# Kernel optimization log

Measured on AMD Instinct MI355X. Metric: run time of the kernel, lower is better.

The kernel has to match this reference:

```python
import jax, jax.numpy as jnp
import numpy as np

N_NODES = 100000
N_EDGES = 1600000
IN_CH = 128
HID = 128
OUT_CH = 40


def setup_inputs() -> dict:
    key = jax.random.key(0)
    ks = jax.random.split(key, 8)
    x = jax.random.normal(ks[0], (N_NODES, IN_CH), dtype=jnp.float32)
    edge_index = jax.random.randint(ks[1], (2, N_EDGES), 0, N_NODES, dtype=jnp.int64)
    s1 = 1.0 / np.sqrt(IN_CH)
    s2 = 1.0 / np.sqrt(HID)
    # SAGEConv layer 1: lin_l (applied to aggregated neighbors, has bias), lin_r (applied to root, no bias)
    Wl1 = jax.random.uniform(ks[2], (IN_CH, HID), jnp.float32, -s1, s1)
    b1 = jnp.zeros((HID,), jnp.float32)
    Wr1 = jax.random.uniform(ks[3], (IN_CH, HID), jnp.float32, -s1, s1)
    # SAGEConv layer 2
    Wl2 = jax.random.uniform(ks[4], (HID, OUT_CH), jnp.float32, -s2, s2)
    b2 = jnp.zeros((OUT_CH,), jnp.float32)
    Wr2 = jax.random.uniform(ks[5], (HID, OUT_CH), jnp.float32, -s2, s2)
    return {"x": x, "edge_index": edge_index, "Wl1": Wl1, "b1": b1, "Wr1": Wr1,
            "Wl2": Wl2, "b2": b2, "Wr2": Wr2}


def _sage_conv(x, src, dst, Wl, b, Wr):
    # mean-aggregate source-node features onto target nodes (PyG SAGEConv, aggr='mean')
    msg_sum = jax.ops.segment_sum(x[src], dst, num_segments=N_NODES)  # [N, F]
    deg = jax.ops.segment_sum(jnp.ones((src.shape[0],), x.dtype), dst, num_segments=N_NODES)
    aggr = msg_sum / jnp.maximum(deg, 1.0)[:, None]
    return aggr @ Wl + b + x @ Wr


def reference(x, edge_index, Wl1, b1, Wr1, Wl2, b2, Wr2):
    src, dst = edge_index[0], edge_index[1]
    h = _sage_conv(x, src, dst, Wl1, b1, Wr1)
    h = jax.nn.relu(h)  # dropout is identity in eval mode
    h = _sage_conv(h, src, dst, Wl2, b2, Wr2)
    return jax.nn.log_softmax(h, axis=-1)
```

## Files before the change

### kernel.cpp

```cpp
#include <hip/hip_runtime.h>
#include <math.h>

#define NN 100000
#define NE 1600000
#define NBUK ((NN + 255) / 256)
#define CAP 5120
#define NBLK_A 500
#define EPB (NE / NBLK_A)
#define GPB (EPB / 4)
#define MT ((NN + 127) / 128)
#define MPAD ((size_t)MT * 128)
#define PACK_B 192
#define CVT_B0 (NBLK_A + PACK_B)
#define FRONT_GRID 2048

typedef __attribute__((ext_vector_type(8))) short short8;
typedef __attribute__((ext_vector_type(4))) float f32x4;
typedef __attribute__((ext_vector_type(4))) int i32x4;
typedef unsigned short ushort_t;
typedef unsigned int uint_t;

__device__ inline ushort_t f2bf(float f) {
    uint_t u = __builtin_bit_cast(uint_t, f);
    u += 0x7FFFu + ((u >> 16) & 1u);
    return (ushort_t)(u >> 16);
}
__device__ inline float bits2f(uint_t u) { return __builtin_bit_cast(float, u); }
__device__ inline float lo16(uint_t u) { return bits2f(u << 16); }
__device__ inline float hi16(uint_t u) { return bits2f(u & 0xFFFF0000u); }

__device__ inline void gload_lds16(const void* g, void* l) {
    __builtin_amdgcn_global_load_lds(
        (const __attribute__((address_space(1))) unsigned int*)g,
        (__attribute__((address_space(3))) unsigned int*)l, 16, 0, 0);
}

__global__ __launch_bounds__(256) void front(const float* __restrict__ x,
                                             ushort_t* __restrict__ xb,
                                             const float* __restrict__ Wl1,
                                             const float* __restrict__ Wr1,
                                             const float* __restrict__ Wl2,
                                             const float* __restrict__ Wr2,
                                             ushort_t* __restrict__ W1T,
                                             ushort_t* __restrict__ W2T,
                                             const int* __restrict__ ei,
                                             int* __restrict__ bhp) {
    __shared__ int h[NBUK];
    int bid = blockIdx.x, tid = threadIdx.x;
    if (bid < NBLK_A) {
        for (int i = tid; i < NBUK; i += 256) h[i] = 0;
        __syncthreads();
        const i32x4* dsts = (const i32x4*)(ei + NE + bid * EPB);
        for (int g = tid; g < GPB; g += 256) {
            i32x4 d = __builtin_nontemporal_load(dsts + g);
#pragma unroll
            for (int j = 0; j < 4; ++j) atomicAdd(&h[d[j] >> 8], 1);
        }
        __syncthreads();
        for (int i = tid; i < NBUK; i += 256) bhp[bid * NBUK + i] = h[i];
    } else if (bid < CVT_B0) {
        int gid = (bid - NBLK_A) * 256 + tid;
        if (gid < 256 * 128) {
            int n = gid >> 7, k = gid & 127;
            float v = (n < 128) ? Wl1[k * 128 + n] : Wr1[k * 128 + (n - 128)];
            W1T[gid] = f2bf(v);
        } else {
            int g = gid - 256 * 128;
            if (g < 128 * 128) {
                int n = g >> 7, k = g & 127;
                float v = 0.0f;
                if (n < 40)      v = Wl2[k * 40 + n];
                else if (n < 80) v = Wr2[k * 40 + (n - 40)];
                W2T[g] = f2bf(v);
            }
        }
    } else {
        const int total = NN * 128 / 8;
        const int nb = FRONT_GRID - CVT_B0;
        const f32x4* src = (const f32x4*)x;
        for (int g = (bid - CVT_B0) * 256 + tid; g < total; g += nb * 256) {
            f32x4 v0 = __builtin_nontemporal_load(src + (size_t)g * 2);
            f32x4 v1 = __builtin_nontemporal_load(src + (size_t)g * 2 + 1);
            i32x4 o;
            o[0] = ((uint_t)f2bf(v0[1]) << 16) | (uint_t)f2bf(v0[0]);
            o[1] = ((uint_t)f2bf(v0[3]) << 16) | (uint_t)f2bf(v0[2]);
            o[2] = ((uint_t)f2bf(v1[1]) << 16) | (uint_t)f2bf(v1[0]);
            o[3] = ((uint_t)f2bf(v1[3]) << 16) | (uint_t)f2bf(v1[2]);
            *(i32x4*)(xb + (size_t)g * 8) = o;
        }
    }
}

__global__ __launch_bounds__(512) void scan_buckets(const int* __restrict__ bhp,
                                                    int* __restrict__ boff,
                                                    int* __restrict__ gcur,
                                                    int* __restrict__ offsets) {
    __shared__ int part[512];
    int t = threadIdx.x;
    int v = 0;
    if (t < NBUK) {
        for (int b = 0; b < NBLK_A; ++b) v += bhp[b * NBUK + t];
    }
    part[t] = v;
    __syncthreads();
    for (int d = 1; d < 512; d <<= 1) {
        int tmp = (t >= d) ? part[t - d] : 0;
        __syncthreads();
        part[t] += tmp;
        __syncthreads();
    }
    if (t <= NBUK) {
        int excl = (t == 0) ? 0 : part[t - 1];
        boff[t] = excl;
        if (t < NBUK) gcur[t] = excl;
    }
    if (t == 0) offsets[NN] = NE;
}

__global__ __launch_bounds__(256) void bin_pass(const int* __restrict__ ei,
                                                const int* __restrict__ bhp,
                                                int* __restrict__ gcur,
                                                int* __restrict__ pairs) {
    __shared__ int h[NBUK];
    __shared__ int base[NBUK];
    int bid = blockIdx.x, tid = threadIdx.x;
    const int* myh = bhp + bid * NBUK;
    for (int i = tid; i < NBUK; i += 256) {
        int c = myh[i];
        base[i] = c ? atomicAdd(&gcur[i], c) : 0;
        h[i] = 0;
    }
    __syncthreads();
    int e0 = bid * EPB;
    const i32x4* dsts = (const i32x4*)(ei + NE + e0);
    const i32x4* srcs = (const i32x4*)(ei + e0);
    for (int g = tid; g < GPB; g += 256) {
        i32x4 d = __builtin_nontemporal_load(dsts + g);
        i32x4 s = __builtin_nontemporal_load(srcs + g);
#pragma unroll
        for (int j = 0; j < 4; ++j) {
            int buk = d[j] >> 8;
            int pos = base[buk] + atomicAdd(&h[buk], 1);
            pairs[pos] = (s[j] << 8) | (d[j] & 255);
        }
    }
}

template <int LAYER>
__device__ inline void gemm_tile(char* As, char* Bs,
                                 const ushort_t* __restrict__ A,
                                 const ushort_t* __restrict__ Bt,
                                 ushort_t* __restrict__ O0,
                                 ushort_t* __restrict__ O1,
                                 ushort_t* __restrict__ Croot,
                                 int bx, int by, int tid, int M) {
    int lane = tid & 63, wid = tid >> 6;
    int quad = lane >> 4, l15 = lane & 15;
    int wm = (wid & 1) * 64, wn = (wid >> 1) * 64;
    int mBase = bx * 128, nBase = by * 128;

    const char* aT = (const char*)(A + (size_t)mBase * 128);
    const char* bT = (const char*)(Bt + (size_t)nBase * 128);
#pragma unroll
    for (int ii = 0; ii < 8; ++ii) {
        int rr = (wid * 8 + ii) * 4 + quad;
        int src = rr * 256 + ((l15 * 16) ^ ((rr & 7) << 4));
        int ldsb = (wid * 8 + ii) * 1024;
        gload_lds16(aT + src, As + ldsb);
        gload_lds16(bT + src, Bs + ldsb);
    }
    asm volatile("s_waitcnt vmcnt(0)" ::: "memory");
    __syncthreads();

    f32x4 acc[4][4];
#pragma unroll
    for (int i = 0; i < 4; ++i)
#pragma unroll
        for (int j = 0; j < 4; ++j) acc[i][j] = (f32x4){0.f, 0.f, 0.f, 0.f};

#pragma unroll
    for (int kk = 0; kk < 4; ++kk) {
        int kByte = kk * 64 + quad * 16;
        short8 af[4], bfr[4];
#pragma unroll
        for (int i = 0; i < 4; ++i) {
            int row = wm + i * 16 + l15;
            af[i] = *(const short8*)(As + row * 256 + (kByte ^ ((row & 7) << 4)));
        }
#pragma unroll
        for (int j = 0; j < 4; ++j) {
            int row = wn + j * 16 + l15;
            bfr[j] = *(const short8*)(Bs + row * 256 + (kByte ^ ((row & 7) << 4)));
        }
#pragma unroll
        for (int i = 0; i < 4; ++i)
#pragma unroll
            for (int j = 0; j < 4; ++j)
                acc[i][j] = __builtin_amdgcn_mfma_f32_16x16x32_bf16(af[i], bfr[j],
                                                                    acc[i][j], 0, 0, 0);
    }

#pragma unroll
    for (int i = 0; i < 4; ++i) {
#pragma unroll
        for (int r = 0; r < 4; ++r) {
            int m = mBase + wm + i * 16 + quad * 4 + r;
            if (m >= M) continue;
#pragma unroll
            for (int j = 0; j < 4; ++j) {
                int n = nBase + wn + j * 16 + l15;
                float v = acc[i][j][r];
                if (LAYER == 1) {
                    if (n < 128) O0[(size_t)m * 128 + n] = f2bf(v);
                    else if (n < 256) Croot[(size_t)m * 128 + (n - 128)] = f2bf(v);
                } else {
                    if (n < 32) O0[(size_t)m * 32 + n] = f2bf(v);
                    else if (n < 40) O1[(size_t)m * 8 + (n - 32)] = f2bf(v);
                    else if (n < 80) Croot[(size_t)m * 40 + (n - 40)] = f2bf(v);
                }
            }
        }
    }
}

__global__ __launch_bounds__(256, 2) void sort_gemm1(const int* __restrict__ boff,
                                                     const int* __restrict__ pairs,
                                                     int* __restrict__ offsets,
                                                     int* __restrict__ ssrc,
                                                     const ushort_t* __restrict__ A,
                                                     const ushort_t* __restrict__ Bt,
                                                     ushort_t* __restrict__ G,
                                                     ushort_t* __restrict__ Croot) {
    __shared__ __align__(16) char smem[65536];
    int bid = blockIdx.x, tid = threadIdx.x;
    if (bid < NBUK) {
        int* plds = (int*)smem;
        int* slds = (int*)(smem + CAP * 4);
        int* cnt  = (int*)(smem + CAP * 8);
        int* excl = cnt + 256;
        int buk = bid;
        int bstart = boff[buk], bend = boff[buk + 1];
        int count = min(bend - bstart, CAP);
        int lo = buk << 8;
        cnt[tid] = 0;
        __syncthreads();
        for (int j = tid; j < count; j += 256) {
            int p = pairs[bstart + j];
            plds[j] = p;
            atomicAdd(&cnt[p & 255], 1);
        }
        __syncthreads();
        int c = cnt[tid];
        excl[tid] = c;
        __syncthreads();
        for (int d = 1; d < 256; d <<= 1) {
            int tmp = (tid >= d) ? excl[tid - d] : 0;
            __syncthreads();
            excl[tid] += tmp;
            __syncthreads();
        }
        int myExcl = excl[tid] - c;
        __syncthreads();
        excl[tid] = myExcl;
        cnt[tid] = 0;
        __syncthreads();
        for (int j = tid; j < count; j += 256) {
            int p = plds[j];
            int loc = p & 255;
            int pos = excl[loc] + atomicAdd(&cnt[loc], 1);
            slds[pos] = p >> 8;
        }
        __syncthreads();
        for (int j = tid; j < count; j += 256) ssrc[bstart + j] = slds[j];
        if (lo + tid < NN) offsets[lo + tid] = bstart + myExcl;
    } else {
        int gb = bid - NBUK;
        int bx = gb % MT, by = gb / MT;
        gemm_tile<1>(smem, smem + 32768, A, Bt, G, (ushort_t*)nullptr, Croot, bx, by, tid, NN);
    }
}

__global__ __launch_bounds__(256, 2) void gemm2_k(const ushort_t* __restrict__ A,
                                                  const ushort_t* __restrict__ Bt,
                                                  ushort_t* __restrict__ G2a,
                                                  ushort_t* __restrict__ G2b,
                                                  ushort_t* __restrict__ C2root) {
    __shared__ __align__(16) char smem[65536];
    gemm_tile<2>(smem, smem + 32768, A, Bt, G2a, G2b, C2root, blockIdx.x, 0, threadIdx.x, NN);
}

__global__ __launch_bounds__(256) void aggregate1(const int* __restrict__ offsets,
                                                  const int* __restrict__ ssrc,
                                                  const ushort_t* __restrict__ G1,
                                                  const ushort_t* __restrict__ C1root,
                                                  const float* __restrict__ b1,
                                                  ushort_t* __restrict__ s1b) {
    int w = (blockIdx.x * blockDim.x + threadIdx.x) >> 6;
    int lane = threadIdx.x & 63;
    if (w >= NN) return;
    int start = offsets[w], end = offsets[w + 1];
    int g = lane >> 4, q = lane & 15;
    const char* Gb = (const char*)G1;
    int qb = q << 4;
    float a0 = 0.f, a1 = 0.f, a2 = 0.f, a3 = 0.f, a4 = 0.f, a5 = 0.f, a6 = 0.f, a7 = 0.f;
    for (int base = start; base < end; base += 64) {
        int cnt = min(64, end - base);
        int idx = (base + lane < end) ? ssrc[base + lane] : 0;
        int j = 0;
        for (; j + 16 <= cnt; j += 16) {
            int s0 = __shfl(idx, j + g, 64);
            int s1 = __shfl(idx, j + 4 + g, 64);
            int s2 = __shfl(idx, j + 8 + g, 64);
            int s3 = __shfl(idx, j + 12 + g, 64);
            uint4 u0 = *(const uint4*)(Gb + (s0 << 8) + qb);
            uint4 u1 = *(const uint4*)(Gb + (s1 << 8) + qb);
            uint4 u2 = *(const uint4*)(Gb + (s2 << 8) + qb);
            uint4 u3 = *(const uint4*)(Gb + (s3 << 8) + qb);
            a0 += (lo16(u0.x) + lo16(u1.x)) + (lo16(u2.x) + lo16(u3.x));
            a1 += (hi16(u0.x) + hi16(u1.x)) + (hi16(u2.x) + hi16(u3.x));
            a2 += (lo16(u0.y) + lo16(u1.y)) + (lo16(u2.y) + lo16(u3.y));
            a3 += (hi16(u0.y) + hi16(u1.y)) + (hi16(u2.y) + hi16(u3.y));
            a4 += (lo16(u0.z) + lo16(u1.z)) + (lo16(u2.z) + lo16(u3.z));
            a5 += (hi16(u0.z) + hi16(u1.z)) + (hi16(u2.z) + hi16(u3.z));
            a6 += (lo16(u0.w) + lo16(u1.w)) + (lo16(u2.w) + lo16(u3.w));
            a7 += (hi16(u0.w) + hi16(u1.w)) + (hi16(u2.w) + hi16(u3.w));
        }
        for (; j + 8 <= cnt; j += 8) {
            int s0 = __shfl(idx, j + g, 64);
            int s1 = __shfl(idx, j + 4 + g, 64);
            uint4 u0 = *(const uint4*)(Gb + (s0 << 8) + qb);
            uint4 u1 = *(const uint4*)(Gb + (s1 << 8) + qb);
            a0 += lo16(u0.x) + lo16(u1.x);
            a1 += hi16(u0.x) + hi16(u1.x);
            a2 += lo16(u0.y) + lo16(u1.y);
            a3 += hi16(u0.y) + hi16(u1.y);
            a4 += lo16(u0.z) + lo16(u1.z);
            a5 += hi16(u0.z) + hi16(u1.z);
            a6 += lo16(u0.w) + lo16(u1.w);
            a7 += hi16(u0.w) + hi16(u1.w);
        }
        for (; j < cnt; j += 4) {
            int e = j + g;
            int s0 = __shfl(idx, (e < cnt) ? e : 0, 64);
            if (e < cnt) {
                uint4 u0 = *(const uint4*)(Gb + (s0 << 8) + qb);
                a0 += lo16(u0.x); a1 += hi16(u0.x);
                a2 += lo16(u0.y); a3 += hi16(u0.y);
                a4 += lo16(u0.z); a5 += hi16(u0.z);
                a6 += lo16(u0.w); a7 += hi16(u0.w);
            }
        }
    }
    a0 += __shfl_xor(a0, 16, 64); a0 += __shfl_xor(a0, 32, 64);
    a1 += __shfl_xor(a1, 16, 64); a1 += __shfl_xor(a1, 32, 64);
    a2 += __shfl_xor(a2, 16, 64); a2 += __shfl_xor(a2, 32, 64);
    a3 += __shfl_xor(a3, 16, 64); a3 += __shfl_xor(a3, 32, 64);
    a4 += __shfl_xor(a4, 16, 64); a4 += __shfl_xor(a4, 32, 64);
    a5 += __shfl_xor(a5, 16, 64); a5 += __shfl_xor(a5, 32, 64);
    a6 += __shfl_xor(a6, 16, 64); a6 += __shfl_xor(a6, 32, 64);
    a7 += __shfl_xor(a7, 16, 64); a7 += __shfl_xor(a7, 32, 64);
    if (g == 0) {
        float inv = 1.0f / fmaxf((float)(end - start), 1.0f);
        uint4 rv = *(const uint4*)((const char*)C1root + (size_t)w * 256 + qb);
        float4 c0 = *(const float4*)(b1 + q * 8);
        float4 c1 = *(const float4*)(b1 + q * 8 + 4);
        float h0 = fmaxf(a0 * inv + c0.x + lo16(rv.x), 0.f);
        float h1 = fmaxf(a1 * inv + c0.y + hi16(rv.x), 0.f);
        float h2 = fmaxf(a2 * inv + c0.z + lo16(rv.y), 0.f);
        float h3 = fmaxf(a3 * inv + c0.w + hi16(rv.y), 0.f);
        float h4 = fmaxf(a4 * inv + c1.x + lo16(rv.z), 0.f);
        float h5 = fmaxf(a5 * inv + c1.y + hi16(rv.z), 0.f);
        float h6 = fmaxf(a6 * inv + c1.z + lo16(rv.w), 0.f);
        float h7 = fmaxf(a7 * inv + c1.w + hi16(rv.w), 0.f);
        uint4 o;
        o.x = ((uint_t)f2bf(h1) << 16) | (uint_t)f2bf(h0);
        o.y = ((uint_t)f2bf(h3) << 16) | (uint_t)f2bf(h2);
        o.z = ((uint_t)f2bf(h5) << 16) | (uint_t)f2bf(h4);
        o.w = ((uint_t)f2bf(h7) << 16) | (uint_t)f2bf(h6);
        *(uint4*)((char*)s1b + (size_t)w * 256 + qb) = o;
    }
}

__global__ __launch_bounds__(256) void aggregate2(const int* __restrict__ offsets,
                                                  const int* __restrict__ ssrc,
                                                  const ushort_t* __restrict__ G2a,
                                                  const ushort_t* __restrict__ G2b,
                                                  const ushort_t* __restrict__ C2root,
                                                  const float* __restrict__ b2,
                                                  float* __restrict__ out) {
    int w = (blockIdx.x * blockDim.x + threadIdx.x) >> 6;
    int lane = threadIdx.x & 63;
    if (w >= NN) return;
    int start = offsets[w], end = offsets[w + 1];
    int g = lane >> 4, q = lane & 15;
    bool act = q < 10;
    const char* tbl;
    int rsh, off0;
    if (q < 8) { tbl = (const char*)G2a; rsh = 6; off0 = q * 8; }
    else       { tbl = (const char*)G2b; rsh = 4; off0 = (q - 8) * 8; }
    float a0 = 0.f, a1 = 0.f, a2 = 0.f, a3 = 0.f;
    for (int base = start; base < end; base += 64) {
        int cnt = min(64, end - base);
        int idx = (base + lane < end) ? ssrc[base + lane] : 0;
        int j = 0;
        for (; j + 16 <= cnt; j += 16) {
            int s0 = __shfl(idx, j + g, 64);
            int s1 = __shfl(idx, j + 4 + g, 64);
            int s2 = __shfl(idx, j + 8 + g, 64);
            int s3 = __shfl(idx, j + 12 + g, 64);
            if (act) {
                uint2 u0 = *(const uint2*)(tbl + ((size_t)s0 << rsh) + off0);
                uint2 u1 = *(const uint2*)(tbl + ((size_t)s1 << rsh) + off0);
                uint2 u2 = *(const uint2*)(tbl + ((size_t)s2 << rsh) + off0);
                uint2 u3 = *(const uint2*)(tbl + ((size_t)s3 << rsh) + off0);
                a0 += (lo16(u0.x) + lo16(u1.x)) + (lo16(u2.x) + lo16(u3.x));
                a1 += (hi16(u0.x) + hi16(u1.x)) + (hi16(u2.x) + hi16(u3.x));
                a2 += (lo16(u0.y) + lo16(u1.y)) + (lo16(u2.y) + lo16(u3.y));
                a3 += (hi16(u0.y) + hi16(u1.y)) + (hi16(u2.y) + hi16(u3.y));
            }
        }
        for (; j + 8 <= cnt; j += 8) {
            int s0 = __shfl(idx, j + g, 64);
            int s1 = __shfl(idx, j + 4 + g, 64);
            if (act) {
                uint2 u0 = *(const uint2*)(tbl + ((size_t)s0 << rsh) + off0);
                uint2 u1 = *(const uint2*)(tbl + ((size_t)s1 << rsh) + off0);
                a0 += lo16(u0.x) + lo16(u1.x);
                a1 += hi16(u0.x) + hi16(u1.x);
                a2 += lo16(u0.y) + lo16(u1.y);
                a3 += hi16(u0.y) + hi16(u1.y);
            }
        }
        for (; j < cnt; j += 4) {
            int e = j + g;
            int s0 = __shfl(idx, (e < cnt) ? e : 0, 64);
            if (act && e < cnt) {
                uint2 u0 = *(const uint2*)(tbl + ((size_t)s0 << rsh) + off0);
                a0 += lo16(u0.x); a1 += hi16(u0.x);
                a2 += lo16(u0.y); a3 += hi16(u0.y);
            }
        }
    }
    a0 += __shfl_xor(a0, 16, 64); a0 += __shfl_xor(a0, 32, 64);
    a1 += __shfl_xor(a1, 16, 64); a1 += __shfl_xor(a1, 32, 64);
    a2 += __shfl_xor(a2, 16, 64); a2 += __shfl_xor(a2, 32, 64);
    a3 += __shfl_xor(a3, 16, 64); a3 += __shfl_xor(a3, 32, 64);
    if (g == 0) {
        float inv = 1.0f / fmaxf((float)(end - start), 1.0f);
        float v0 = -INFINITY, v1 = -INFINITY, v2 = -INFINITY, v3 = -INFINITY;
        if (act) {
            uint2 rv = *(const uint2*)((const char*)C2root + (size_t)w * 80 + (q << 3));
            float4 bb = *(const float4*)(b2 + q * 4);
            v0 = a0 * inv + bb.x + lo16(rv.x);
            v1 = a1 * inv + bb.y + hi16(rv.x);
            v2 = a2 * inv + bb.z + lo16(rv.y);
            v3 = a3 * inv + bb.w + hi16(rv.y);
        }
        float m = fmaxf(fmaxf(v0, v1), fmaxf(v2, v3));
#pragma unroll
        for (int d = 8; d >= 1; d >>= 1) m = fmaxf(m, __shfl_xor(m, d, 64));
        float e = act ? (expf(v0 - m) + expf(v1 - m)) + (expf(v2 - m) + expf(v3 - m)) : 0.f;
#pragma unroll
        for (int d = 8; d >= 1; d >>= 1) e += __shfl_xor(e, d, 64);
        float lse = m + logf(e);
        if (act) {
            float4 o = make_float4(v0 - lse, v1 - lse, v2 - lse, v3 - lse);
            *(float4*)(out + (size_t)w * 40 + q * 4) = o;
        }
    }
}

extern "C" void kernel_launch(void* const* d_in, const int* in_sizes, int n_in,
                              void* d_out, int out_size, void* d_ws, size_t ws_size,
                              hipStream_t stream) {
    const float* x   = (const float*)d_in[0];
    const int*   ei  = (const int*)d_in[1];
    const float* Wl1 = (const float*)d_in[2];
    const float* b1  = (const float*)d_in[3];
    const float* Wr1 = (const float*)d_in[4];
    const float* Wl2 = (const float*)d_in[5];
    const float* b2  = (const float*)d_in[6];
    const float* Wr2 = (const float*)d_in[7];
    float* out = (float*)d_out;

    char* ws = (char*)d_ws;
    size_t off = 0;
    auto alloc = [&](size_t bytes) -> void* {
        void* p = ws + off;
        off = (off + bytes + 255) & ~(size_t)255;
        return p;
    };
    int*      boff    = (int*)alloc((size_t)(NBUK + 1) * 4);
    int*      gcur    = (int*)alloc((size_t)NBUK * 4);
    int*      bhp     = (int*)alloc((size_t)NBLK_A * NBUK * 4);
    int*      pairs   = (int*)alloc((size_t)NE * 4);
    int*      offsets = (int*)alloc((size_t)(NN + 1) * 4);
    int*      ssrc    = (int*)alloc((size_t)NE * 4);
    ushort_t* W1T     = (ushort_t*)alloc((size_t)256 * 128 * 2);
    ushort_t* W2T     = (ushort_t*)alloc((size_t)128 * 128 * 2);
    ushort_t* xb      = (ushort_t*)alloc(MPAD * 128 * 2);
    ushort_t* G1      = (ushort_t*)alloc((size_t)NN * 128 * 2);
    ushort_t* C1root  = (ushort_t*)alloc((size_t)NN * 128 * 2);
    ushort_t* s1b     = (ushort_t*)alloc(MPAD * 128 * 2);
    ushort_t* G2a     = (ushort_t*)alloc((size_t)NN * 32 * 2);
    ushort_t* G2b     = (ushort_t*)alloc((size_t)NN * 8 * 2);
    ushort_t* C2root  = (ushort_t*)alloc((size_t)NN * 40 * 2);

    front<<<FRONT_GRID, 256, 0, stream>>>(x, xb, Wl1, Wr1, Wl2, Wr2, W1T, W2T, ei, bhp);
    scan_buckets<<<1, 512, 0, stream>>>(bhp, boff, gcur, offsets);
    bin_pass<<<NBLK_A, 256, 0, stream>>>(ei, bhp, gcur, pairs);
    sort_gemm1<<<NBUK + MT * 2, 256, 0, stream>>>(boff, pairs, offsets, ssrc,
                                                  xb, W1T, G1, C1root);
    aggregate1<<<(NN * 64 + 255) / 256, 256, 0, stream>>>(offsets, ssrc, G1, C1root, b1, s1b);
    gemm2_k<<<MT, 256, 0, stream>>>(s1b, W2T, G2a, G2b, C2root);
    aggregate2<<<(NN * 64 + 255) / 256, 256, 0, stream>>>(offsets, ssrc, G2a, G2b,
                                                          C2root, b2, out);
}
```

Baseline: 326.8 us.

## Use fixed-capacity buckets and fuse layer-2 GEMM into aggregation

Edge binning now gives each bucket a fixed-capacity region (bucket*CAP). This drops the global histogram pass in front and the single-block scan kernel, and bin_pass computes its own per-block histogram. Node ranges are stored as separate start/end arrays. The layer-2 GEMM kernel is removed: each wavefront multiplies its aggregated hidden row by W2 with scalar FMAs and shuffles, which avoids writing and re-reading s1b. The cost is that edges beyond a bucket's CAP are silently dropped, and the per-node dot products on CUDA cores replace the MFMA GEMM.

```diff
diff --git a/kernel.cpp b/kernel.cpp
--- a/kernel.cpp
+++ b/kernel.cpp
@@ -11,7 +11,6 @@
 #define MT ((NN + 127) / 128)
 #define MPAD ((size_t)MT * 128)
 #define PACK_B 192
-#define CVT_B0 (NBLK_A + PACK_B)
 #define FRONT_GRID 2048
 
 typedef __attribute__((ext_vector_type(8))) short short8;
@@ -28,6 +27,7 @@
 __device__ inline float bits2f(uint_t u) { return __builtin_bit_cast(float, u); }
 __device__ inline float lo16(uint_t u) { return bits2f(u << 16); }
 __device__ inline float hi16(uint_t u) { return bits2f(u & 0xFFFF0000u); }
+__device__ inline float bf2f(ushort_t b) { return bits2f((uint_t)b << 16); }
 
 __device__ inline void gload_lds16(const void* g, void* l) {
     __builtin_amdgcn_global_load_lds(
@@ -43,23 +43,13 @@
                                              const float* __restrict__ Wr2,
                                              ushort_t* __restrict__ W1T,
                                              ushort_t* __restrict__ W2T,
-                                             const int* __restrict__ ei,
-                                             int* __restrict__ bhp) {
-    __shared__ int h[NBUK];
+                                             int* __restrict__ gcur) {
     int bid = blockIdx.x, tid = threadIdx.x;
-    if (bid < NBLK_A) {
-        for (int i = tid; i < NBUK; i += 256) h[i] = 0;
-        __syncthreads();
-        const i32x4* dsts = (const i32x4*)(ei + NE + bid * EPB);
-        for (int g = tid; g < GPB; g += 256) {
-            i32x4 d = __builtin_nontemporal_load(dsts + g);
-#pragma unroll
-            for (int j = 0; j < 4; ++j) atomicAdd(&h[d[j] >> 8], 1);
-        }
-        __syncthreads();
-        for (int i = tid; i < NBUK; i += 256) bhp[bid * NBUK + i] = h[i];
-    } else if (bid < CVT_B0) {
-        int gid = (bid - NBLK_A) * 256 + tid;
+    if (bid == 0) {
+        for (int i = tid; i < NBUK; i += 256) gcur[i] = i * CAP;
+    }
+    if (bid < PACK_B) {
+        int gid = bid * 256 + tid;
         if (gid < 256 * 128) {
             int n = gid >> 7, k = gid & 127;
             float v = (n < 128) ? Wl1[k * 128 + n] : Wr1[k * 128 + (n - 128)];
@@ -76,9 +66,9 @@
         }
     } else {
         const int total = NN * 128 / 8;
-        const int nb = FRONT_GRID - CVT_B0;
+        const int nb = FRONT_GRID - PACK_B;
         const f32x4* src = (const f32x4*)x;
-        for (int g = (bid - CVT_B0) * 256 + tid; g < total; g += nb * 256) {
+        for (int g = (bid - PACK_B) * 256 + tid; g < total; g += nb * 256) {
             f32x4 v0 = __builtin_nontemporal_load(src + (size_t)g * 2);
             f32x4 v1 = __builtin_nontemporal_load(src + (size_t)g * 2 + 1);
             i32x4 o;
@@ -91,69 +81,47 @@
     }
 }
 
-__global__ __launch_bounds__(512) void scan_buckets(const int* __restrict__ bhp,
-                                                    int* __restrict__ boff,
-                                                    int* __restrict__ gcur,
-                                                    int* __restrict__ offsets) {
-    __shared__ int part[512];
-    int t = threadIdx.x;
-    int v = 0;
-    if (t < NBUK) {
-        for (int b = 0; b < NBLK_A; ++b) v += bhp[b * NBUK + t];
-    }
-    part[t] = v;
-    __syncthreads();
-    for (int d = 1; d < 512; d <<= 1) {
-        int tmp = (t >= d) ? part[t - d] : 0;
-        __syncthreads();
-        part[t] += tmp;
-        __syncthreads();
-    }
-    if (t <= NBUK) {
-        int excl = (t == 0) ? 0 : part[t - 1];
-        boff[t] = excl;
-        if (t < NBUK) gcur[t] = excl;
-    }
-    if (t == 0) offsets[NN] = NE;
-}
-
 __global__ __launch_bounds__(256) void bin_pass(const int* __restrict__ ei,
-                                                const int* __restrict__ bhp,
                                                 int* __restrict__ gcur,
                                                 int* __restrict__ pairs) {
     __shared__ int h[NBUK];
     __shared__ int base[NBUK];
     int bid = blockIdx.x, tid = threadIdx.x;
-    const int* myh = bhp + bid * NBUK;
-    for (int i = tid; i < NBUK; i += 256) {
-        int c = myh[i];
-        base[i] = c ? atomicAdd(&gcur[i], c) : 0;
-        h[i] = 0;
-    }
+    for (int i = tid; i < NBUK; i += 256) h[i] = 0;
     __syncthreads();
     int e0 = bid * EPB;
     const i32x4* dsts = (const i32x4*)(ei + NE + e0);
     const i32x4* srcs = (const i32x4*)(ei + e0);
     for (int g = tid; g < GPB; g += 256) {
         i32x4 d = __builtin_nontemporal_load(dsts + g);
+#pragma unroll
+        for (int j = 0; j < 4; ++j) atomicAdd(&h[d[j] >> 8], 1);
+    }
+    __syncthreads();
+    for (int i = tid; i < NBUK; i += 256) {
+        int c = h[i];
+        base[i] = c ? atomicAdd(&gcur[i], c) : 0;
+        h[i] = 0;
+    }
+    __syncthreads();
+    for (int g = tid; g < GPB; g += 256) {
+        i32x4 d = __builtin_nontemporal_load(dsts + g);
         i32x4 s = __builtin_nontemporal_load(srcs + g);
 #pragma unroll
         for (int j = 0; j < 4; ++j) {
             int buk = d[j] >> 8;
             int pos = base[buk] + atomicAdd(&h[buk], 1);
-            pairs[pos] = (s[j] << 8) | (d[j] & 255);
-        }
-    }
-}
-
-template <int LAYER>
-__device__ inline void gemm_tile(char* As, char* Bs,
-                                 const ushort_t* __restrict__ A,
-                                 const ushort_t* __restrict__ Bt,
-                                 ushort_t* __restrict__ O0,
-                                 ushort_t* __restrict__ O1,
-                                 ushort_t* __restrict__ Croot,
-                                 int bx, int by, int tid, int M) {
+            if (pos < (buk + 1) * CAP) pairs[pos] = (s[j] << 8) | (d[j] & 255);
+        }
+    }
+}
+
+__device__ inline void gemm1_tile(char* As, char* Bs,
+                                  const ushort_t* __restrict__ A,
+                                  const ushort_t* __restrict__ Bt,
+                                  ushort_t* __restrict__ G,
+                                  ushort_t* __restrict__ Croot,
+                                  int bx, int by, int tid) {
     int lane = tid & 63, wid = tid >> 6;
     int quad = lane >> 4, l15 = lane & 15;
     int wm = (wid & 1) * 64, wn = (wid >> 1) * 64;
@@ -205,27 +173,22 @@
 #pragma unroll
         for (int r = 0; r < 4; ++r) {
             int m = mBase + wm + i * 16 + quad * 4 + r;
-            if (m >= M) continue;
+            if (m >= NN) continue;
 #pragma unroll
             for (int j = 0; j < 4; ++j) {
                 int n = nBase + wn + j * 16 + l15;
                 float v = acc[i][j][r];
-                if (LAYER == 1) {
-                    if (n < 128) O0[(size_t)m * 128 + n] = f2bf(v);
-                    else if (n < 256) Croot[(size_t)m * 128 + (n - 128)] = f2bf(v);
-                } else {
-                    if (n < 32) O0[(size_t)m * 32 + n] = f2bf(v);
-                    else if (n < 40) O1[(size_t)m * 8 + (n - 32)] = f2bf(v);
-                    else if (n < 80) Croot[(size_t)m * 40 + (n - 40)] = f2bf(v);
-                }
-            }
-        }
-    }
-}
-
-__global__ __launch_bounds__(256, 2) void sort_gemm1(const int* __restrict__ boff,
+                if (n < 128) G[(size_t)m * 128 + n] = f2bf(v);
+                else Croot[(size_t)m * 128 + (n - 128)] = f2bf(v);
+            }
+        }
+    }
+}
+
+__global__ __launch_bounds__(256, 2) void sort_gemm1(const int* __restrict__ gcur,
                                                      const int* __restrict__ pairs,
-                                                     int* __restrict__ offsets,
+                                                     int* __restrict__ starts,
+                                                     int* __restrict__ ends,
                                                      int* __restrict__ ssrc,
                                                      const ushort_t* __restrict__ A,
                                                      const ushort_t* __restrict__ Bt,
@@ -239,8 +202,8 @@
         int* cnt  = (int*)(smem + CAP * 8);
         int* excl = cnt + 256;
         int buk = bid;
-        int bstart = boff[buk], bend = boff[buk + 1];
-        int count = min(bend - bstart, CAP);
+        int bstart = buk * CAP;
+        int count = min(gcur[buk] - bstart, CAP);
         int lo = buk << 8;
         cnt[tid] = 0;
         __syncthreads();
@@ -272,33 +235,31 @@
         }
         __syncthreads();
         for (int j = tid; j < count; j += 256) ssrc[bstart + j] = slds[j];
-        if (lo + tid < NN) offsets[lo + tid] = bstart + myExcl;
+        if (lo + tid < NN) {
+            starts[lo + tid] = bstart + myExcl;
+            ends[lo + tid]   = bstart + myExcl + c;
+        }
     } else {
         int gb = bid - NBUK;
         int bx = gb % MT, by = gb / MT;
-        gemm_tile<1>(smem, smem + 32768, A, Bt, G, (ushort_t*)nullptr, Croot, bx, by, tid, NN);
-    }
-}
-
-__global__ __launch_bounds__(256, 2) void gemm2_k(const ushort_t* __restrict__ A,
-                                                  const ushort_t* __restrict__ Bt,
-                                                  ushort_t* __restrict__ G2a,
-                                                  ushort_t* __restrict__ G2b,
-                                                  ushort_t* __restrict__ C2root) {
-    __shared__ __align__(16) char smem[65536];
-    gemm_tile<2>(smem, smem + 32768, A, Bt, G2a, G2b, C2root, blockIdx.x, 0, threadIdx.x, NN);
-}
-
-__global__ __launch_bounds__(256) void aggregate1(const int* __restrict__ offsets,
-                                                  const int* __restrict__ ssrc,
-                                                  const ushort_t* __restrict__ G1,
-                                                  const ushort_t* __restrict__ C1root,
-                                                  const float* __restrict__ b1,
-                                                  ushort_t* __restrict__ s1b) {
+        gemm1_tile(smem, smem + 32768, A, Bt, G, Croot, bx, by, tid);
+    }
+}
+
+__global__ __launch_bounds__(256) void aggregate1f(const int* __restrict__ starts,
+                                                   const int* __restrict__ ends,
+                                                   const int* __restrict__ ssrc,
+                                                   const ushort_t* __restrict__ G1,
+                                                   const ushort_t* __restrict__ C1root,
+                                                   const float* __restrict__ b1,
+                                                   const ushort_t* __restrict__ W2T,
+                                                   ushort_t* __restrict__ G2a,
+                                                   ushort_t* __restrict__ G2b,
+                                                   ushort_t* __restrict__ C2root) {
     int w = (blockIdx.x * blockDim.x + threadIdx.x) >> 6;
     int lane = threadIdx.x & 63;
     if (w >= NN) return;
-    int start = offsets[w], end = offsets[w + 1];
+    int start = starts[w], end = ends[w];
     int g = lane >> 4, q = lane & 15;
     const char* Gb = (const char*)G1;
     int qb = q << 4;
@@ -359,29 +320,48 @@
     a5 += __shfl_xor(a5, 16, 64); a5 += __shfl_xor(a5, 32, 64);
     a6 += __shfl_xor(a6, 16, 64); a6 += __shfl_xor(a6, 32, 64);
     a7 += __shfl_xor(a7, 16, 64); a7 += __shfl_xor(a7, 32, 64);
-    if (g == 0) {
-        float inv = 1.0f / fmaxf((float)(end - start), 1.0f);
-        uint4 rv = *(const uint4*)((const char*)C1root + (size_t)w * 256 + qb);
-        float4 c0 = *(const float4*)(b1 + q * 8);
-        float4 c1 = *(const float4*)(b1 + q * 8 + 4);
-        float h0 = fmaxf(a0 * inv + c0.x + lo16(rv.x), 0.f);
-        float h1 = fmaxf(a1 * inv + c0.y + hi16(rv.x), 0.f);
-        float h2 = fmaxf(a2 * inv + c0.z + lo16(rv.y), 0.f);
-        float h3 = fmaxf(a3 * inv + c0.w + hi16(rv.y), 0.f);
-        float h4 = fmaxf(a4 * inv + c1.x + lo16(rv.z), 0.f);
-        float h5 = fmaxf(a5 * inv + c1.y + hi16(rv.z), 0.f);
-        float h6 = fmaxf(a6 * inv + c1.z + lo16(rv.w), 0.f);
-        float h7 = fmaxf(a7 * inv + c1.w + hi16(rv.w), 0.f);
-        uint4 o;
-        o.x = ((uint_t)f2bf(h1) << 16) | (uint_t)f2bf(h0);
-        o.y = ((uint_t)f2bf(h3) << 16) | (uint_t)f2bf(h2);
-        o.z = ((uint_t)f2bf(h5) << 16) | (uint_t)f2bf(h4);
-        o.w = ((uint_t)f2bf(h7) << 16) | (uint_t)f2bf(h6);
-        *(uint4*)((char*)s1b + (size_t)w * 256 + qb) = o;
-    }
-}
-
-__global__ __launch_bounds__(256) void aggregate2(const int* __restrict__ offsets,
+
+    float inv = 1.0f / fmaxf((float)(end - start), 1.0f);
+    uint4 rv = *(const uint4*)((const char*)C1root + (size_t)w * 256 + qb);
+    float4 c0 = *(const float4*)(b1 + q * 8);
+    float4 c1 = *(const float4*)(b1 + q * 8 + 4);
+    float hf0 = bf2f(f2bf(fmaxf(a0 * inv + c0.x + lo16(rv.x), 0.f)));
+    float hf1 = bf2f(f2bf(fmaxf(a1 * inv + c0.y + hi16(rv.x), 0.f)));
+    float hf2 = bf2f(f2bf(fmaxf(a2 * inv + c0.z + lo16(rv.y), 0.f)));
+    float hf3 = bf2f(f2bf(fmaxf(a3 * inv + c0.w + hi16(rv.y), 0.f)));
+    float hf4 = bf2f(f2bf(fmaxf(a4 * inv + c1.x + lo16(rv.z), 0.f)));
+    float hf5 = bf2f(f2bf(fmaxf(a5 * inv + c1.y + hi16(rv.z), 0.f)));
+    float hf6 = bf2f(f2bf(fmaxf(a6 * inv + c1.z + lo16(rv.w), 0.f)));
+    float hf7 = bf2f(f2bf(fmaxf(a7 * inv + c1.w + hi16(rv.w), 0.f)));
+
+    float accL = 0.f, accH = 0.f;
+    const ushort_t* WrowL = W2T + (size_t)lane * 128;
+    const ushort_t* WrowH = W2T + (size_t)(64 + q) * 128;
+#pragma unroll
+    for (int kq = 0; kq < 16; ++kq) {
+        float hb0 = __shfl(hf0, kq, 64), hb1 = __shfl(hf1, kq, 64);
+        float hb2 = __shfl(hf2, kq, 64), hb3 = __shfl(hf3, kq, 64);
+        float hb4 = __shfl(hf4, kq, 64), hb5 = __shfl(hf5, kq, 64);
+        float hb6 = __shfl(hf6, kq, 64), hb7 = __shfl(hf7, kq, 64);
+        short8 wl = *(const short8*)(WrowL + kq * 8);
+        short8 wh = *(const short8*)(WrowH + kq * 8);
+        accL += hb0 * bf2f((ushort_t)wl[0]) + hb1 * bf2f((ushort_t)wl[1])
+              + hb2 * bf2f((ushort_t)wl[2]) + hb3 * bf2f((ushort_t)wl[3])
+              + hb4 * bf2f((ushort_t)wl[4]) + hb5 * bf2f((ushort_t)wl[5])
+              + hb6 * bf2f((ushort_t)wl[6]) + hb7 * bf2f((ushort_t)wl[7]);
+        accH += hb0 * bf2f((ushort_t)wh[0]) + hb1 * bf2f((ushort_t)wh[1])
+              + hb2 * bf2f((ushort_t)wh[2]) + hb3 * bf2f((ushort_t)wh[3])
+              + hb4 * bf2f((ushort_t)wh[4]) + hb5 * bf2f((ushort_t)wh[5])
+              + hb6 * bf2f((ushort_t)wh[6]) + hb7 * bf2f((ushort_t)wh[7]);
+    }
+    if (lane < 32) G2a[(size_t)w * 32 + lane] = f2bf(accL);
+    else if (lane < 40) G2b[(size_t)w * 8 + (lane - 32)] = f2bf(accL);
+    else C2root[(size_t)w * 40 + (lane - 40)] = f2bf(accL);
+    if (lane < 16) C2root[(size_t)w * 40 + 24 + lane] = f2bf(accH);
+}
+
+__global__ __launch_bounds__(256) void aggregate2(const int* __restrict__ starts,
+                                                  const int* __restrict__ ends,
                                                   const int* __restrict__ ssrc,
                                                   const ushort_t* __restrict__ G2a,
                                                   const ushort_t* __restrict__ G2b,
@@ -391,7 +371,7 @@
     int w = (blockIdx.x * blockDim.x + threadIdx.x) >> 6;
     int lane = threadIdx.x & 63;
     if (w >= NN) return;
-    int start = offsets[w], end = offsets[w + 1];
+    int start = starts[w], end = ends[w];
     int g = lane >> 4, q = lane & 15;
     bool act = q < 10;
     const char* tbl;
@@ -490,29 +470,26 @@
         off = (off + bytes + 255) & ~(size_t)255;
         return p;
     };
-    int*      boff    = (int*)alloc((size_t)(NBUK + 1) * 4);
     int*      gcur    = (int*)alloc((size_t)NBUK * 4);
-    int*      bhp     = (int*)alloc((size_t)NBLK_A * NBUK * 4);
-    int*      pairs   = (int*)alloc((size_t)NE * 4);
-    int*      offsets = (int*)alloc((size_t)(NN + 1) * 4);
-    int*      ssrc    = (int*)alloc((size_t)NE * 4);
+    int*      pairs   = (int*)alloc((size_t)NBUK * CAP * 4);
+    int*      starts  = (int*)alloc((size_t)NN * 4);
+    int*      ends    = (int*)alloc((size_t)NN * 4);
+    int*      ssrc    = (int*)alloc((size_t)NBUK * CAP * 4);
     ushort_t* W1T     = (ushort_t*)alloc((size_t)256 * 128 * 2);
     ushort_t* W2T     = (ushort_t*)alloc((size_t)128 * 128 * 2);
     ushort_t* xb      = (ushort_t*)alloc(MPAD * 128 * 2);
     ushort_t* G1      = (ushort_t*)alloc((size_t)NN * 128 * 2);
     ushort_t* C1root  = (ushort_t*)alloc((size_t)NN * 128 * 2);
-    ushort_t* s1b     = (ushort_t*)alloc(MPAD * 128 * 2);
     ushort_t* G2a     = (ushort_t*)alloc((size_t)NN * 32 * 2);
     ushort_t* G2b     = (ushort_t*)alloc((size_t)NN * 8 * 2);
     ushort_t* C2root  = (ushort_t*)alloc((size_t)NN * 40 * 2);
 
-    front<<<FRONT_GRID, 256, 0, stream>>>(x, xb, Wl1, Wr1, Wl2, Wr2, W1T, W2T, ei, bhp);
-    scan_buckets<<<1, 512, 0, stream>>>(bhp, boff, gcur, offsets);
-    bin_pass<<<NBLK_A, 256, 0, stream>>>(ei, bhp, gcur, pairs);
-    sort_gemm1<<<NBUK + MT * 2, 256, 0, stream>>>(boff, pairs, offsets, ssrc,
+    front<<<FRONT_GRID, 256, 0, stream>>>(x, xb, Wl1, Wr1, Wl2, Wr2, W1T, W2T, gcur);
+    bin_pass<<<NBLK_A, 256, 0, stream>>>(ei, gcur, pairs);
+    sort_gemm1<<<NBUK + MT * 2, 256, 0, stream>>>(gcur, pairs, starts, ends, ssrc,
                                                   xb, W1T, G1, C1root);
-    aggregate1<<<(NN * 64 + 255) / 256, 256, 0, stream>>>(offsets, ssrc, G1, C1root, b1, s1b);
-    gemm2_k<<<MT, 256, 0, stream>>>(s1b, W2T, G2a, G2b, C2root);
-    aggregate2<<<(NN * 64 + 255) / 256, 256, 0, stream>>>(offsets, ssrc, G2a, G2b,
+    aggregate1f<<<(NN * 64 + 255) / 256, 256, 0, stream>>>(starts, ends, ssrc, G1, C1root,
+                                                           b1, W2T, G2a, G2b, C2root);
+    aggregate2<<<(NN * 64 + 255) / 256, 256, 0, stream>>>(starts, ends, ssrc, G2a, G2b,
                                                           C2root, b2, out);
 }
```

After: 647.3 us. +98.1%, slower.
